# Kernel tuning notes

Measured on AMD Instinct MI355X. Metric: run time of the kernel, lower is better.

The kernel has to match this reference:

```python
import jax, jax.numpy as jnp
import numpy as np

D = 1024
H = 16
HD = D // H
COND = 128
MLP = 4 * D
B, S = 4, 1024
LN_EPS = 1e-5


def _layer_norm(x, w):
    # fp32 LayerNorm (no bias), then scale by weight, matching custom LayerNorm
    xf = x.astype(jnp.float32)
    mu = jnp.mean(xf, axis=-1, keepdims=True)
    var = jnp.mean(jnp.square(xf - mu), axis=-1, keepdims=True)
    y = (xf - mu) * jax.lax.rsqrt(var + LN_EPS)
    return y * w[None, None, :]


def _modulate(x, shift, scale):
    # shift/scale: [B, D] -> broadcast over seq
    return x * (1.0 + scale[:, None, :]) + shift[:, None, :]


def _rope(t, cos, sin):
    # t: [B,S,H,hd]; cos/sin: [S, hd//2]  (GPT-NeoX half-split rotary)
    c = cos[None, :, None, :]
    s = sin[None, :, None, :]
    t1, t2 = jnp.split(t, 2, axis=-1)
    return jnp.concatenate([t1 * c - t2 * s, t2 * c + t1 * s], axis=-1)


def setup_inputs() -> dict:
    key = jax.random.key(0)
    ks = jax.random.split(key, 12)
    std = 0.02
    inp = {
        "x": jax.random.normal(ks[0], (B, S, D), dtype=jnp.float32),
        "c": jax.random.normal(ks[1], (B, COND), dtype=jnp.float32),
        "norm1_w": jnp.ones((D,), dtype=jnp.float32),
        "norm2_w": jnp.ones((D,), dtype=jnp.float32),
        "w_qkv": jax.random.normal(ks[2], (D, 3 * D), dtype=jnp.float32) * std,
        "w_out": jax.random.normal(ks[3], (D, D), dtype=jnp.float32) * std,
        "w1": jax.random.normal(ks[4], (D, MLP), dtype=jnp.float32) * std,
        "b1": jnp.zeros((MLP,), dtype=jnp.float32),
        "w2": jax.random.normal(ks[5], (MLP, D), dtype=jnp.float32) * std,
        "b2": jnp.zeros((D,), dtype=jnp.float32),
        "adaLN_w": jax.random.normal(ks[6], (COND, 6 * D), dtype=jnp.float32) * std,
        "adaLN_b": jnp.zeros((6 * D,), dtype=jnp.float32),
    }
    # rotary tables: cos/sin [S, hd//2]
    inv_freq = 1.0 / (10000.0 ** (jnp.arange(0, HD, 2, dtype=jnp.float32) / HD))
    t = jnp.arange(S, dtype=jnp.float32)
    freqs = t[:, None] * inv_freq[None, :]  # [S, hd//2]
    inp["cos"] = jnp.cos(freqs)
    inp["sin"] = jnp.sin(freqs)
    return inp


def reference(x, c, norm1_w, norm2_w, w_qkv, w_out, w1, b1, w2, b2, adaLN_w, adaLN_b, cos, sin):
    b, s, d = x.shape
    hd = 2 * cos.shape[-1]
    h = d // hd

    # adaLN modulation -> 6 chunks of [B, D]
    mod = c @ adaLN_w + adaLN_b
    shift_msa, scale_msa, gate_msa, shift_mlp, scale_mlp, gate_mlp = jnp.split(mod, 6, axis=-1)

    x_skip = x
    xm = _modulate(_layer_norm(x, norm1_w), shift_msa, scale_msa)

    qkv = (xm @ w_qkv).reshape(b, s, 3, h, hd)
    q = _rope(qkv[:, :, 0], cos, sin)
    k = _rope(qkv[:, :, 1], cos, sin)
    v = qkv[:, :, 2]

    scale = 1.0 / jnp.sqrt(jnp.asarray(hd, dtype=x.dtype))
    scores = jnp.einsum("bshd,bthd->bhst", q, k) * scale
    probs = jax.nn.softmax(scores, axis=-1)
    attn = jnp.einsum("bhst,bthd->bshd", probs, v).reshape(b, s, d)

    # bias_dropout_add_scale (inference: dropout off): residual + gate * out
    x = x_skip + gate_msa[:, None, :] * (attn @ w_out)

    xm2 = _modulate(_layer_norm(x, norm2_w), shift_mlp, scale_mlp)
    hdn = jax.nn.gelu(xm2 @ w1 + b1, approximate=True)
    mlp_out = hdn @ w2 + b2
    x = x + gate_mlp[:, None, :] * mlp_out
    return x
```

## Files before the change

### kernel.cpp

```cpp
#include <hip/hip_runtime.h>

typedef unsigned short u16;
typedef unsigned int u32;
typedef short bf16x8 __attribute__((ext_vector_type(8)));
typedef float f32x4 __attribute__((ext_vector_type(4)));

#define DD 1024
#define SS 1024
#define HH 16
#define HDIM 64
#define MODW 6144

__device__ __forceinline__ float b2f(u16 h){ u32 u = ((u32)h)<<16; return __builtin_bit_cast(float,u); }
__device__ __forceinline__ u16 f2b(float f){
  u32 u = __builtin_bit_cast(u32,f);
  return (u16)((u + 0x7fffu + ((u>>16)&1u))>>16);
}
__device__ __forceinline__ u32 cvtpk(float a, float b){
  u32 r; asm("v_cvt_pk_bf16_f32 %0, %1, %2" : "=v"(r) : "v"(a), "v"(b)); return r;
}
__device__ __forceinline__ void gload16(const u16* g, u16* l){
  __builtin_amdgcn_global_load_lds((const __attribute__((address_space(1))) void*)g,
                                   (__attribute__((address_space(3))) void*)l, 16, 0, 0);
}

__global__ void k_zero(float* __restrict__ out){
  int i = blockIdx.x*256 + threadIdx.x;
  ((float4*)out)[i] = make_float4(0.f,0.f,0.f,0.f);
}

__device__ __forceinline__ void tcast_tile(const float* in, u16* out, int K, int N, int bx, int by){
  __shared__ float t[32][33];
  int n0 = bx*32, k0 = by*32;
  int tx = threadIdx.x & 31, ty = threadIdx.x >> 5;
  #pragma unroll
  for (int i=0;i<4;i++){
    int k = k0 + ty + i*8;
    t[ty+i*8][tx] = in[(size_t)k*N + n0 + tx];
  }
  __syncthreads();
  #pragma unroll
  for (int i=0;i<4;i++){
    int n = n0 + ty + i*8;
    out[(size_t)n*K + k0 + tx] = f2b(t[tx][ty+i*8]);
  }
}
__global__ void k_prep(const float* __restrict__ wqkv, const float* __restrict__ wout,
                       const float* __restrict__ w1, const float* __restrict__ w2,
                       u16* __restrict__ wqkvT, u16* __restrict__ woutT,
                       u16* __restrict__ w1T, u16* __restrict__ w2T,
                       const float* __restrict__ c, const float* __restrict__ aw,
                       const float* __restrict__ ab, float* __restrict__ mod){
  int bid = blockIdx.x;
  if (bid < 3072)       tcast_tile(wqkv, wqkvT, 1024, 3072, bid%96,  bid/96);
  else if (bid < 4096){ int t=bid-3072; tcast_tile(wout, woutT, 1024, 1024, t%32, t/32); }
  else if (bid < 8192){ int t=bid-4096; tcast_tile(w1,   w1T,   1024, 4096, t%128,t/128); }
  else if (bid < 12288){int t=bid-8192; tcast_tile(w2,   w2T,   4096, 1024, t%32, t/32); }
  else {
    int t = bid - 12288;
    int n = (t%24)*256 + threadIdx.x;
    int bb = t/24;
    float acc = ab[n];
    #pragma unroll 4
    for (int k=0;k<128;k++) acc += c[bb*128+k]*aw[(size_t)k*MODW + n];
    mod[(size_t)bb*MODW + n] = acc;
  }
}

__global__ void k_ln_mod(const float* __restrict__ x, const float* __restrict__ w,
                         const float* __restrict__ mod, int shc, int scc,
                         u16* __restrict__ out){
  int row = blockIdx.x;
  int b = row >> 10;
  const float* xr = x + (size_t)row*DD;
  float4 v = ((const float4*)xr)[threadIdx.x];
  float s = v.x+v.y+v.z+v.w;
  float sq = v.x*v.x+v.y*v.y+v.z*v.z+v.w*v.w;
  #pragma unroll
  for (int o=32;o;o>>=1){ s += __shfl_xor(s,o); sq += __shfl_xor(sq,o); }
  __shared__ float ls[4], lq[4];
  int wid = threadIdx.x>>6, lane = threadIdx.x&63;
  if (lane==0){ ls[wid]=s; lq[wid]=sq; }
  __syncthreads();
  s = ls[0]+ls[1]+ls[2]+ls[3]; sq = lq[0]+lq[1]+lq[2]+lq[3];
  float mu = s*(1.f/DD);
  float var = sq*(1.f/DD) - mu*mu;
  float rs = rsqrtf(var + 1e-5f);
  int d0 = threadIdx.x*4;
  const float* mb = mod + (size_t)b*MODW;
  float y0 = ((v.x-mu)*rs*w[d0+0])*(1.f+mb[scc+d0+0]) + mb[shc+d0+0];
  float y1 = ((v.y-mu)*rs*w[d0+1])*(1.f+mb[scc+d0+1]) + mb[shc+d0+1];
  float y2 = ((v.z-mu)*rs*w[d0+2])*(1.f+mb[scc+d0+2]) + mb[shc+d0+2];
  float y3 = ((v.w-mu)*rs*w[d0+3])*(1.f+mb[scc+d0+3]) + mb[shc+d0+3];
  uint2 pk;
  pk.x = (u32)f2b(y0) | ((u32)f2b(y1)<<16);
  pk.y = (u32)f2b(y2) | ((u32)f2b(y3)<<16);
  ((uint2*)(out + (size_t)row*DD))[threadIdx.x] = pk;
}

enum { EPI_QKV=0, EPI_GELU=2, EPI_PARTB=5 };

template<int EPI>
__launch_bounds__(512, 2)
__global__ void k_gemm256(const u16* __restrict__ A, const u16* __restrict__ Bt,
                          int M, int N, int K, int kstride,
                          const float* __restrict__ bias,
                          u16* __restrict__ outb,
                          const float* __restrict__ cosb, const float* __restrict__ sinb,
                          u16* __restrict__ qh, u16* __restrict__ kh, u16* __restrict__ vt){
  __shared__ __align__(16) u16 lds[4][2][8192];
  int tid = threadIdx.x, lane = tid & 63;
  int wid = tid >> 6, wr = wid >> 2, wc = wid & 3;
  int bm = blockIdx.x*256, bn = blockIdx.y*256, z = blockIdx.z;
  f32x4 acc[8][4] = {};
  int srow = (tid>>6)*16 + (tid&15);
  int skk  = ((tid>>4)&3)*8;
  const u16* pa = A  + (size_t)(bm+srow)*kstride + (size_t)z*K + skk;
  const u16* pb = Bt + (size_t)(bn+srow)*kstride + (size_t)z*K + skk;
  size_t rh = (size_t)128*kstride;
  int nk = K >> 5;
  #pragma unroll
  for (int t=0; t<3; ++t){
    gload16(pa + t*32,      &lds[t][0][tid*8]);
    gload16(pa + rh + t*32, &lds[t][0][4096 + tid*8]);
    gload16(pb + t*32,      &lds[t][1][tid*8]);
    gload16(pb + rh + t*32, &lds[t][1][4096 + tid*8]);
  }
  for (int t=0; t<nk; ++t){
    const u16* lA = &lds[t&3][0][0];
    const u16* lB = &lds[t&3][1][0];
    int ahead = nk-1-t;
    if (ahead >= 2)      asm volatile("s_waitcnt vmcnt(8)" ::: "memory");
    else if (ahead == 1) asm volatile("s_waitcnt vmcnt(4)" ::: "memory");
    else                 asm volatile("s_waitcnt vmcnt(0)" ::: "memory");
    __builtin_amdgcn_s_barrier();
    __builtin_amdgcn_sched_barrier(0);
    if (t+3 < nk){
      int u = t+3;
      gload16(pa + u*32,      &lds[u&3][0][tid*8]);
      gload16(pa + rh + u*32, &lds[u&3][0][4096 + tid*8]);
      gload16(pb + u*32,      &lds[u&3][1][tid*8]);
      gload16(pb + rh + u*32, &lds[u&3][1][4096 + tid*8]);
    }
    __builtin_amdgcn_s_setprio(1);
    bf16x8 fa[8], fb[4];
    #pragma unroll
    for (int mi=0;mi<8;mi++) fa[mi] = *(const bf16x8*)(lA + ((wr*8+mi)*64 + lane)*8);
    #pragma unroll
    for (int ni=0;ni<4;ni++) fb[ni] = *(const bf16x8*)(lB + ((wc*4+ni)*64 + lane)*8);
    #pragma unroll
    for (int mi=0;mi<8;mi++)
      #pragma unroll
      for (int ni=0;ni<4;ni++)
        acc[mi][ni] = __builtin_amdgcn_mfma_f32_16x16x32_bf16(fa[mi], fb[ni], acc[mi][ni], 0,0,0);
    __builtin_amdgcn_s_setprio(0);
  }
  int ln = lane & 15;
  int rbase = bm + wr*128 + ((lane>>4)<<2);
  if (EPI == EPI_QKV){
    int cbg = bn + wc*64;
    int ii = cbg >> 10;
    int hh = (cbg >> 6) & 15;
    if (ii == 2){
      #pragma unroll
      for (int mi=0;mi<8;mi++){
        int row = rbase + mi*16;
        int s = row & 1023, b = row >> 10;
        size_t ob = (size_t)(b*16+hh)*65536;
        #pragma unroll
        for (int ni=0;ni<4;ni++){
          int d = ni*16 + ln;
          u32 lo = (u32)f2b(acc[mi][ni][0]) | ((u32)f2b(acc[mi][ni][1])<<16);
          u32 hi = (u32)f2b(acc[mi][ni][2]) | ((u32)f2b(acc[mi][ni][3])<<16);
          *(uint2*)(vt + ob + (size_t)d*1024 + s) = make_uint2(lo,hi);
        }
      }
    } else {
      u16* dst = (ii==0) ? qh : kh;
      float qs = (ii==0) ? 0.125f : 1.0f;
      #pragma unroll
      for (int mi=0;mi<8;mi++){
        #pragma unroll
        for (int r=0;r<4;r++){
          int row = rbase + mi*16 + r;
          int s = row & 1023, b = row >> 10;
          size_t ob = ((size_t)(b*16+hh)*1024 + s)*64;
          #pragma unroll
          for (int ni=0;ni<2;ni++){
            int dlow = ni*16 + ln;
            float cc = cosb[s*32 + dlow], sn = sinb[s*32 + dlow];
            float t1 = acc[mi][ni][r], t2 = acc[mi][ni+2][r];
            dst[ob + dlow]      = f2b((t1*cc - t2*sn)*qs);
            dst[ob + dlow + 32] = f2b((t2*cc + t1*sn)*qs);
          }
        }
      }
    }
    return;
  }
  if (EPI == EPI_PARTB){
    u16* po = outb + (size_t)z*M*N;
    #pragma unroll
    for (int mi=0;mi<8;mi++)
      #pragma unroll
      for (int ni=0;ni<4;ni++){
        int col = bn + wc*64 + ni*16 + ln;
        #pragma unroll
        for (int r=0;r<4;r++)
          po[(size_t)(rbase+mi*16+r)*N + col] = f2b(acc[mi][ni][r]);
      }
    return;
  }
  #pragma unroll
  for (int mi=0;mi<8;mi++)
    #pragma unroll
    for (int ni=0;ni<4;ni++){
      int col = bn + wc*64 + ni*16 + ln;
      float bb = bias[col];
      #pragma unroll
      for (int r=0;r<4;r++){
        float t = acc[mi][ni][r] + bb;
        float y = 0.7978845608f*(t + 0.044715f*t*t*t);
        y = fminf(fmaxf(y, -15.f), 15.f);
        float e = __expf(2.f*y);
        float g = 0.5f*t*(1.f + (e-1.f)/(e+1.f));
        outb[(size_t)(rbase+mi*16+r)*N + col] = f2b(g);
      }
    }
}

__global__ void k_red_ln(const u16* __restrict__ part, const float* __restrict__ x,
                         const float* __restrict__ mod, const float* __restrict__ w,
                         float* __restrict__ x2, u16* __restrict__ act){
  int row = blockIdx.x;
  int b = row >> 10;
  int tid = threadIdx.x;
  int col = tid*4;
  size_t base = (size_t)row*DD + col;
  const size_t MN = (size_t)4096*1024;
  float4 ps = make_float4(0.f,0.f,0.f,0.f);
  #pragma unroll
  for (int z=0; z<4; z++){
    uint2 p = *(const uint2*)(part + (size_t)z*MN + base);
    ps.x += b2f((u16)p.x); ps.y += b2f((u16)(p.x>>16));
    ps.z += b2f((u16)p.y); ps.w += b2f((u16)(p.y>>16));
  }
  const float* mb = mod + (size_t)b*MODW;
  float4 g = *(const float4*)(mb + 2*DD + col);
  float4 rr = *(const float4*)(x + base);
  float4 v;
  v.x = rr.x + g.x*ps.x;
  v.y = rr.y + g.y*ps.y;
  v.z = rr.z + g.z*ps.z;
  v.w = rr.w + g.w*ps.w;
  *(float4*)(x2 + base) = v;
  float s = v.x+v.y+v.z+v.w;
  float sq = v.x*v.x+v.y*v.y+v.z*v.z+v.w*v.w;
  #pragma unroll
  for (int o=32;o;o>>=1){ s += __shfl_xor(s,o); sq += __shfl_xor(sq,o); }
  __shared__ float ls[4], lq[4];
  int wid = tid>>6, lane = tid&63;
  if (lane==0){ ls[wid]=s; lq[wid]=sq; }
  __syncthreads();
  s = ls[0]+ls[1]+ls[2]+ls[3]; sq = lq[0]+lq[1]+lq[2]+lq[3];
  float mu = s*(1.f/DD);
  float var = sq*(1.f/DD) - mu*mu;
  float rs = rsqrtf(var + 1e-5f);
  float y0 = ((v.x-mu)*rs*w[col+0])*(1.f+mb[4*DD+col+0]) + mb[3*DD+col+0];
  float y1 = ((v.y-mu)*rs*w[col+1])*(1.f+mb[4*DD+col+1]) + mb[3*DD+col+1];
  float y2 = ((v.z-mu)*rs*w[col+2])*(1.f+mb[4*DD+col+2]) + mb[3*DD+col+2];
  float y3 = ((v.w-mu)*rs*w[col+3])*(1.f+mb[4*DD+col+3]) + mb[3*DD+col+3];
  uint2 pk;
  pk.x = (u32)f2b(y0) | ((u32)f2b(y1)<<16);
  pk.y = (u32)f2b(y2) | ((u32)f2b(y3)<<16);
  *(uint2*)(act + base) = pk;
}

__global__ void k_reduce4b(const u16* __restrict__ part, size_t MN,
                           const float* __restrict__ resid,
                           const float* __restrict__ mod, int gate_off,
                           const float* __restrict__ bias,
                           float* __restrict__ out){
  int i = blockIdx.x*256 + threadIdx.x;
  int e = i<<2;
  int col = e & 1023;
  int row = e >> 10;
  int b = row >> 10;
  float4 s = make_float4(0.f,0.f,0.f,0.f);
  #pragma unroll
  for (int z=0; z<4; z++){
    uint2 p = ((const uint2*)(part + (size_t)z*MN))[i];
    s.x += b2f((u16)p.x); s.y += b2f((u16)(p.x>>16));
    s.z += b2f((u16)p.y); s.w += b2f((u16)(p.y>>16));
  }
  float4 bb = *(const float4*)(bias + col);
  s.x+=bb.x; s.y+=bb.y; s.z+=bb.z; s.w+=bb.w;
  float4 g = *(const float4*)(mod + (size_t)b*MODW + gate_off + col);
  float4 rr = ((const float4*)resid)[i];
  float4 o;
  o.x = rr.x + g.x*s.x; o.y = rr.y + g.y*s.y;
  o.z = rr.z + g.z*s.z; o.w = rr.w + g.w*s.w;
  ((float4*)out)[i] = o;
}

__launch_bounds__(256, 4)
__global__ void k_attn(const u16* __restrict__ qh, const u16* __restrict__ kh,
                       const u16* __restrict__ vt, u16* __restrict__ attn){
  int blk = blockIdx.x;
  int bh = blk >> 4;
  int qt = blk & 15;
  int tid = threadIdx.x, lane = tid&63, wid = tid>>6;
  int ln = lane&15, kg = lane>>4;
  int sw = ln & 7;
  __shared__ __align__(16) u16 KV[2][2][4096];
  const size_t hb = (size_t)bh*SS*HDIM;

  int qrow = qt*64 + wid*16 + ln;
  const u16* qp = qh + hb + (size_t)qrow*64 + kg*8;
  bf16x8 qf0 = *(const bf16x8*)qp;
  bf16x8 qf1 = *(const bf16x8*)(qp + 32);

  int w0i = wid*64 + lane, w1i = w0i + 256;
  int r0 = w0i>>3, sl0 = (w0i&7) ^ (r0&7);
  int r1 = w1i>>3, sl1 = (w1i&7) ^ (r1&7);
  const u16* gk0 = kh + hb + (size_t)r0*64 + sl0*8;
  const u16* gk1 = kh + hb + (size_t)r1*64 + sl1*8;
  const u16* gv0 = vt + hb + (size_t)r0*1024 + sl0*8;
  const u16* gv1 = vt + hb + (size_t)r1*1024 + sl1*8;

  float mrun = -1e30f, lrun = 0.f;
  f32x4 oc[4] = {};

  gload16(gk0, &KV[0][0][w0i*8]);
  gload16(gk1, &KV[0][0][w1i*8]);
  gload16(gv0, &KV[0][1][w0i*8]);
  gload16(gv1, &KV[0][1][w1i*8]);

  for (int kt=0; kt<16; ++kt){
    int buf = kt & 1;
    __builtin_amdgcn_s_barrier();
    asm volatile("" ::: "memory");
    if (kt < 15){
      int u = kt+1;
      gload16(gk0 + u*4096, &KV[buf^1][0][w0i*8]);
      gload16(gk1 + u*4096, &KV[buf^1][0][w1i*8]);
      gload16(gv0 + u*64,   &KV[buf^1][1][w0i*8]);
      gload16(gv1 + u*64,   &KV[buf^1][1][w1i*8]);
      asm volatile("s_waitcnt vmcnt(4)" ::: "memory");
    } else {
      asm volatile("s_waitcnt vmcnt(0)" ::: "memory");
    }
    __builtin_amdgcn_s_barrier();
    const u16* Kb = KV[buf][0];
    const u16* Vb = KV[buf][1];

    f32x4 sc[4];
    #pragma unroll
    for (int c=0;c<4;c++){
      const u16* kr = Kb + (c*16+ln)*64;
      bf16x8 kf0 = *(const bf16x8*)(kr + (((kg  )^sw)<<3));
      bf16x8 kf1 = *(const bf16x8*)(kr + (((kg+4)^sw)<<3));
      f32x4 zz = {};
      zz   = __builtin_amdgcn_mfma_f32_16x16x32_bf16(kf0, qf0, zz, 0,0,0);
      sc[c]= __builtin_amdgcn_mfma_f32_16x16x32_bf16(kf1, qf1, zz, 0,0,0);
    }
    float mx = fmaxf(fmaxf(fmaxf(sc[0][0],sc[0][1]),fmaxf(sc[0][2],sc[0][3])),
                     fmaxf(fmaxf(sc[1][0],sc[1][1]),fmaxf(sc[1][2],sc[1][3])));
    float mx2= fmaxf(fmaxf(fmaxf(sc[2][0],sc[2][1]),fmaxf(sc[2][2],sc[2][3])),
                     fmaxf(fmaxf(sc[3][0],sc[3][1]),fmaxf(sc[3][2],sc[3][3])));
    mx = fmaxf(mx, mx2);
    mx = fmaxf(mx, __shfl_xor(mx, 16));
    mx = fmaxf(mx, __shfl_xor(mx, 32));
    float mn = fmaxf(mrun, mx);
    float al = __expf(mrun - mn);
    mrun = mn;
    u32 pk[4][2];
    float sum = 0.f;
    #pragma unroll
    for (int c=0;c<4;c++){
      float p0 = __expf(sc[c][0]-mn), p1 = __expf(sc[c][1]-mn);
      float p2 = __expf(sc[c][2]-mn), p3 = __expf(sc[c][3]-mn);
      sum += (p0+p1)+(p2+p3);
      pk[c][0] = cvtpk(p0,p1);
      pk[c][1] = cvtpk(p2,p3);
    }
    sum += __shfl_xor(sum, 16);
    sum += __shfl_xor(sum, 32);
    lrun = lrun*al + sum;
    float alr0 = __shfl(al, kg*4+0), alr1 = __shfl(al, kg*4+1);
    float alr2 = __shfl(al, kg*4+2), alr3 = __shfl(al, kg*4+3);
    #pragma unroll
    for (int c=0;c<4;c++){ oc[c][0]*=alr0; oc[c][1]*=alr1; oc[c][2]*=alr2; oc[c][3]*=alr3; }
    int srcA = ((kg&1)<<5) + ln;
    int hi = kg >> 1;
    #pragma unroll
    for (int kc=0;kc<2;kc++){
      u32 a0 = (u32)__shfl((int)pk[2*kc  ][0], srcA   ), b0 = (u32)__shfl((int)pk[2*kc+1][0], srcA   );
      u32 a1 = (u32)__shfl((int)pk[2*kc  ][1], srcA   ), b1 = (u32)__shfl((int)pk[2*kc+1][1], srcA   );
      u32 a2 = (u32)__shfl((int)pk[2*kc  ][0], srcA+16), b2 = (u32)__shfl((int)pk[2*kc+1][0], srcA+16);
      u32 a3 = (u32)__shfl((int)pk[2*kc  ][1], srcA+16), b3 = (u32)__shfl((int)pk[2*kc+1][1], srcA+16);
      uint4 wv = make_uint4(hi? b0:a0, hi? b1:a1, hi? b2:a2, hi? b3:a3);
      bf16x8 af = __builtin_bit_cast(bf16x8, wv);
      #pragma unroll
      for (int c=0;c<4;c++){
        const u16* vr = Vb + (c*16+ln)*64;
        bf16x8 vf = *(const bf16x8*)(vr + (((kg+4*kc)^sw)<<3));
        oc[c] = __builtin_amdgcn_mfma_f32_16x16x32_bf16(af, vf, oc[c], 0,0,0);
      }
    }
  }
  int b = bh >> 4, h = bh & 15;
  float linv[4];
  linv[0] = 1.f/__shfl(lrun, kg*4+0); linv[1] = 1.f/__shfl(lrun, kg*4+1);
  linv[2] = 1.f/__shfl(lrun, kg*4+2); linv[3] = 1.f/__shfl(lrun, kg*4+3);
  #pragma unroll
  for (int r=0;r<4;r++){
    int srow = qt*64 + wid*16 + kg*4 + r;
    u16* op = attn + (size_t)(b*1024+srow)*DD + h*64;
    #pragma unroll
    for (int c=0;c<4;c++) op[c*16+ln] = f2b(oc[c][r]*linv[r]);
  }
}

extern "C" void kernel_launch(void* const* d_in, const int* in_sizes, int n_in,
                              void* d_out, int out_size, void* d_ws, size_t ws_size,
                              hipStream_t stream){
  const float* x   = (const float*)d_in[0];
  const float* c   = (const float*)d_in[1];
  const float* n1w = (const float*)d_in[2];
  const float* n2w = (const float*)d_in[3];
  const float* wqkv= (const float*)d_in[4];
  const float* wout= (const float*)d_in[5];
  const float* w1  = (const float*)d_in[6];
  const float* b1  = (const float*)d_in[7];
  const float* w2  = (const float*)d_in[8];
  const float* b2  = (const float*)d_in[9];
  const float* aw  = (const float*)d_in[10];
  const float* ab  = (const float*)d_in[11];
  const float* cosb= (const float*)d_in[12];
  const float* sinb= (const float*)d_in[13];

  const size_t REQ = 117538816;
  if (ws_size < REQ){
    k_zero<<<4096,256,0,stream>>>((float*)d_out);
    return;
  }
  char* ws = (char*)d_ws;
  u16*   wqkvT = (u16*)(ws + 0);
  u16*   woutT = (u16*)(ws + 6291456);
  u16*   act   = (u16*)(ws + 8388608);
  float* mod   = (float*)(ws + 16777216);
  float* x2    = (float*)(ws + 16875520);
  u16*   qh    = (u16*)(ws + 16875520);
  u16*   kh    = (u16*)(ws + 25264128);
  u16*   vt    = (u16*)(ws + 33652736);
  u16*   part2b= (u16*)(ws + 33652736);
  u16*   hbuf  = (u16*)(ws + 33652736);
  u16*   w1T   = (u16*)(ws + 67207168);
  u16*   w2T   = (u16*)(ws + 75595776);
  u16*   part4b= (u16*)(ws + 83984384);

  k_prep<<<12384,256,0,stream>>>(wqkv, wout, w1, w2, wqkvT, woutT, w1T, w2T, c, aw, ab, mod);
  k_ln_mod<<<4096,256,0,stream>>>(x, n1w, mod, 0*DD, 1*DD, act);
  k_gemm256<EPI_QKV ><<<dim3(16,12,1),512,0,stream>>>(act, wqkvT, 4096,3072,1024,1024,
        nullptr, nullptr, cosb, sinb, qh, kh, vt);
  k_attn<<<1024,256,0,stream>>>(qh, kh, vt, act);
  k_gemm256<EPI_PARTB><<<dim3(16,4,4),512,0,stream>>>(act, woutT, 4096,1024,256,1024,
        nullptr, part2b, nullptr, nullptr, nullptr, nullptr, nullptr);
  k_red_ln<<<4096,256,0,stream>>>(part2b, x, mod, n2w, x2, act);
  k_gemm256<EPI_GELU><<<dim3(16,16,1),512,0,stream>>>(act, w1T, 4096,4096,1024,1024,
        b1, hbuf, nullptr, nullptr, nullptr, nullptr, nullptr);
  k_gemm256<EPI_PARTB><<<dim3(16,4,4),512,0,stream>>>(hbuf, w2T, 4096,1024,1024,4096,
        nullptr, part4b, nullptr, nullptr, nullptr, nullptr, nullptr);
  k_reduce4b<<<4096,256,0,stream>>>(part4b, (size_t)4096*1024, x2, mod, 5*DD, b2, (float*)d_out);
}
```

Baseline: 362.8 us.

## Restructure GEMM main loop into double-buffered 4-phase interleaved load/MFMA schedule

Replaces the 4-stage LDS ring buffer (one K=32 slice per stage) in the 256x256 GEMM with double-buffered K=64 tiles split into separate A and B buffers. Each K tile is processed in four phases that interleave LDS fragment reads, next-tile global-to-LDS loads, and quarter-sized MFMA bursts with explicit barriers and waitcnts. The aim is to overlap memory traffic with MFMA work at finer granularity and cut register pressure for fragments. It adds many more barriers per iteration and a shallower prefetch depth, which could expose global load latency.

```diff
diff --git a/kernel.cpp b/kernel.cpp
--- a/kernel.cpp
+++ b/kernel.cpp
@@ -100,6 +100,33 @@
 
 enum { EPI_QKV=0, EPI_GELU=2, EPI_PARTB=5 };
 
+#define BARR  __builtin_amdgcn_s_barrier()
+#define LGKM0 asm volatile("s_waitcnt lgkmcnt(0)" ::: "memory")
+#define SB0   __builtin_amdgcn_sched_barrier(0)
+#define VMC(n) asm volatile("s_waitcnt vmcnt(" #n ")" ::: "memory")
+
+#define STG_A(bf, kt, kh) do{ const u16* _s = pa + (kt)*64 + (kh)*32; \
+  gload16(_s,      &Als[bf][kh][tid*8]); \
+  gload16(_s + rh, &Als[bf][kh][(512+tid)*8]); }while(0)
+#define STG_B(bf, kt, kh) do{ const u16* _s = pb + (kt)*64 + (kh)*32; \
+  gload16(_s,      &Bls[bf][kh][tid*8]); \
+  gload16(_s + rh, &Bls[bf][kh][(512+tid)*8]); }while(0)
+
+#define LDA4(bf, kh, mlo) do{ const u16* _b = &Als[bf][kh][0]; \
+  _Pragma("unroll") \
+  for (int m=0;m<4;m++) av[m] = *(const bf16x8*)(_b + ((wr*8+(mlo)+m)*64 + lane)*8); }while(0)
+#define LDB4(bf, kh) do{ const u16* _b = &Bls[bf][kh][0]; \
+  _Pragma("unroll") \
+  for (int n=0;n<4;n++) bv[n] = *(const bf16x8*)(_b + ((wc*4+n)*64 + lane)*8); }while(0)
+
+#define MMQ4(mlo) do{ __builtin_amdgcn_s_setprio(1); \
+  _Pragma("unroll") \
+  for (int m=0;m<4;m++){ \
+    _Pragma("unroll") \
+    for (int n=0;n<4;n++) \
+      acc[(mlo)+m][n] = __builtin_amdgcn_mfma_f32_16x16x32_bf16(av[m], bv[n], acc[(mlo)+m][n], 0,0,0); } \
+  __builtin_amdgcn_s_setprio(0); }while(0)
+
 template<int EPI>
 __launch_bounds__(512, 2)
 __global__ void k_gemm256(const u16* __restrict__ A, const u16* __restrict__ Bt,
@@ -108,7 +135,8 @@
                           u16* __restrict__ outb,
                           const float* __restrict__ cosb, const float* __restrict__ sinb,
                           u16* __restrict__ qh, u16* __restrict__ kh, u16* __restrict__ vt){
-  __shared__ __align__(16) u16 lds[4][2][8192];
+  __shared__ __align__(16) u16 Als[2][2][8192];
+  __shared__ __align__(16) u16 Bls[2][2][8192];
   int tid = threadIdx.x, lane = tid & 63;
   int wid = tid >> 6, wr = wid >> 2, wc = wid & 3;
   int bm = blockIdx.x*256, bn = blockIdx.y*256, z = blockIdx.z;
@@ -118,42 +146,41 @@
   const u16* pa = A  + (size_t)(bm+srow)*kstride + (size_t)z*K + skk;
   const u16* pb = Bt + (size_t)(bn+srow)*kstride + (size_t)z*K + skk;
   size_t rh = (size_t)128*kstride;
-  int nk = K >> 5;
-  #pragma unroll
-  for (int t=0; t<3; ++t){
-    gload16(pa + t*32,      &lds[t][0][tid*8]);
-    gload16(pa + rh + t*32, &lds[t][0][4096 + tid*8]);
-    gload16(pb + t*32,      &lds[t][1][tid*8]);
-    gload16(pb + rh + t*32, &lds[t][1][4096 + tid*8]);
-  }
-  for (int t=0; t<nk; ++t){
-    const u16* lA = &lds[t&3][0][0];
-    const u16* lB = &lds[t&3][1][0];
-    int ahead = nk-1-t;
-    if (ahead >= 2)      asm volatile("s_waitcnt vmcnt(8)" ::: "memory");
-    else if (ahead == 1) asm volatile("s_waitcnt vmcnt(4)" ::: "memory");
-    else                 asm volatile("s_waitcnt vmcnt(0)" ::: "memory");
-    __builtin_amdgcn_s_barrier();
-    __builtin_amdgcn_sched_barrier(0);
-    if (t+3 < nk){
-      int u = t+3;
-      gload16(pa + u*32,      &lds[u&3][0][tid*8]);
-      gload16(pa + rh + u*32, &lds[u&3][0][4096 + tid*8]);
-      gload16(pb + u*32,      &lds[u&3][1][tid*8]);
-      gload16(pb + rh + u*32, &lds[u&3][1][4096 + tid*8]);
-    }
-    __builtin_amdgcn_s_setprio(1);
-    bf16x8 fa[8], fb[4];
-    #pragma unroll
-    for (int mi=0;mi<8;mi++) fa[mi] = *(const bf16x8*)(lA + ((wr*8+mi)*64 + lane)*8);
-    #pragma unroll
-    for (int ni=0;ni<4;ni++) fb[ni] = *(const bf16x8*)(lB + ((wc*4+ni)*64 + lane)*8);
-    #pragma unroll
-    for (int mi=0;mi<8;mi++)
-      #pragma unroll
-      for (int ni=0;ni<4;ni++)
-        acc[mi][ni] = __builtin_amdgcn_mfma_f32_16x16x32_bf16(fa[mi], fb[ni], acc[mi][ni], 0,0,0);
-    __builtin_amdgcn_s_setprio(0);
+  int nkt = K >> 6;
+  bf16x8 av[4], bv[4];
+
+  STG_A(0, 0, 0);
+  STG_B(0, 0, 0);
+  STG_A(0, 0, 1);
+  STG_B(0, 0, 1);
+  VMC(4);
+  BARR; SB0;
+
+  for (int kt=0; kt<nkt; ++kt){
+    int bf = kt & 1;
+    bool nx = (kt+1 < nkt);
+    LDA4(bf, 0, 0); LDB4(bf, 0);
+    if (nx) STG_A(bf^1, kt+1, 0);
+    BARR; LGKM0; SB0;
+    MMQ4(0);
+    BARR; SB0;
+    LDA4(bf, 0, 4);
+    if (nx) STG_B(bf^1, kt+1, 0);
+    BARR; LGKM0; SB0;
+    MMQ4(4);
+    if (nx) VMC(4); else VMC(0);
+    BARR; SB0;
+    LDA4(bf, 1, 0); LDB4(bf, 1);
+    if (nx) STG_A(bf^1, kt+1, 1);
+    BARR; LGKM0; SB0;
+    MMQ4(0);
+    BARR; SB0;
+    LDA4(bf, 1, 4);
+    if (nx) STG_B(bf^1, kt+1, 1);
+    BARR; LGKM0; SB0;
+    MMQ4(4);
+    if (nx) VMC(4);
+    BARR; SB0;
   }
   int ln = lane & 15;
   int rbase = bm + wr*128 + ((lane>>4)<<2);
```

New measurement: 374.2 us. 1.03x slower.

## Shrink GEMM tile to 256x128 with XCD-aware block remap and 3-stage buffer

Applied to the files above, without the earlier changes.

The shared GEMM kernel drops from a 256x256 tile to 256x128, with each wave holding a 64x64 accumulator instead of 128x64. The LDS pipeline goes from 4 stages to 3, and launch bounds now request 4 blocks per SM. Block indices are remapped so that neighbouring tiles land on the same XCD, which should improve L2 reuse. This doubles the grid sizes and aims for more occupancy and better tail balance, at the cost of lower arithmetic intensity per tile and a shallower prefetch.

```diff
diff --git a/kernel.cpp b/kernel.cpp
--- a/kernel.cpp
+++ b/kernel.cpp
@@ -100,70 +100,74 @@
 
 enum { EPI_QKV=0, EPI_GELU=2, EPI_PARTB=5 };
 
+#define VMC(n) asm volatile("s_waitcnt vmcnt(" #n ")" ::: "memory")
+
 template<int EPI>
-__launch_bounds__(512, 2)
+__launch_bounds__(512, 4)
 __global__ void k_gemm256(const u16* __restrict__ A, const u16* __restrict__ Bt,
                           int M, int N, int K, int kstride,
                           const float* __restrict__ bias,
                           u16* __restrict__ outb,
                           const float* __restrict__ cosb, const float* __restrict__ sinb,
                           u16* __restrict__ qh, u16* __restrict__ kh, u16* __restrict__ vt){
-  __shared__ __align__(16) u16 lds[4][2][8192];
+  __shared__ __align__(16) u16 Ab[3][8192];
+  __shared__ __align__(16) u16 Bb[3][4096];
   int tid = threadIdx.x, lane = tid & 63;
-  int wid = tid >> 6, wr = wid >> 2, wc = wid & 3;
-  int bm = blockIdx.x*256, bn = blockIdx.y*256, z = blockIdx.z;
-  f32x4 acc[8][4] = {};
+  int wid = tid >> 6, wr = wid >> 1, wc = wid & 1;
+  int g   = blockIdx.y * gridDim.x + blockIdx.x;
+  int xcd = g & 7, slot = g >> 3;
+  int gy2 = gridDim.y >> 1;
+  int bxp = (xcd >> 1)*4 + (slot & 3);
+  int byp = (xcd & 1)*gy2 + (slot >> 2);
+  int bm = bxp*256, bn = byp*128, z = blockIdx.z;
+  f32x4 acc[4][4] = {};
   int srow = (tid>>6)*16 + (tid&15);
   int skk  = ((tid>>4)&3)*8;
   const u16* pa = A  + (size_t)(bm+srow)*kstride + (size_t)z*K + skk;
   const u16* pb = Bt + (size_t)(bn+srow)*kstride + (size_t)z*K + skk;
   size_t rh = (size_t)128*kstride;
   int nk = K >> 5;
-  #pragma unroll
-  for (int t=0; t<3; ++t){
-    gload16(pa + t*32,      &lds[t][0][tid*8]);
-    gload16(pa + rh + t*32, &lds[t][0][4096 + tid*8]);
-    gload16(pb + t*32,      &lds[t][1][tid*8]);
-    gload16(pb + rh + t*32, &lds[t][1][4096 + tid*8]);
-  }
+  gload16(pa,           &Ab[0][tid*8]);
+  gload16(pa + rh,      &Ab[0][(512+tid)*8]);
+  gload16(pb,           &Bb[0][tid*8]);
+  gload16(pa + 32,      &Ab[1][tid*8]);
+  gload16(pa + rh + 32, &Ab[1][(512+tid)*8]);
+  gload16(pb + 32,      &Bb[1][tid*8]);
   for (int t=0; t<nk; ++t){
-    const u16* lA = &lds[t&3][0][0];
-    const u16* lB = &lds[t&3][1][0];
-    int ahead = nk-1-t;
-    if (ahead >= 2)      asm volatile("s_waitcnt vmcnt(8)" ::: "memory");
-    else if (ahead == 1) asm volatile("s_waitcnt vmcnt(4)" ::: "memory");
-    else                 asm volatile("s_waitcnt vmcnt(0)" ::: "memory");
+    if (t+1 < nk) VMC(3); else VMC(0);
     __builtin_amdgcn_s_barrier();
     __builtin_amdgcn_sched_barrier(0);
-    if (t+3 < nk){
-      int u = t+3;
-      gload16(pa + u*32,      &lds[u&3][0][tid*8]);
-      gload16(pa + rh + u*32, &lds[u&3][0][4096 + tid*8]);
-      gload16(pb + u*32,      &lds[u&3][1][tid*8]);
-      gload16(pb + rh + u*32, &lds[u&3][1][4096 + tid*8]);
-    }
+    if (t+2 < nk){
+      int bf = (t+2)%3;
+      const u16* s = pa + (t+2)*32;
+      gload16(s,              &Ab[bf][tid*8]);
+      gload16(s + rh,         &Ab[bf][(512+tid)*8]);
+      gload16(pb + (t+2)*32,  &Bb[bf][tid*8]);
+    }
+    const u16* lA = &Ab[t%3][0];
+    const u16* lB = &Bb[t%3][0];
     __builtin_amdgcn_s_setprio(1);
-    bf16x8 fa[8], fb[4];
-    #pragma unroll
-    for (int mi=0;mi<8;mi++) fa[mi] = *(const bf16x8*)(lA + ((wr*8+mi)*64 + lane)*8);
+    bf16x8 fa[4], fb[4];
+    #pragma unroll
+    for (int mi=0;mi<4;mi++) fa[mi] = *(const bf16x8*)(lA + ((wr*4+mi)*64 + lane)*8);
     #pragma unroll
     for (int ni=0;ni<4;ni++) fb[ni] = *(const bf16x8*)(lB + ((wc*4+ni)*64 + lane)*8);
     #pragma unroll
-    for (int mi=0;mi<8;mi++)
+    for (int mi=0;mi<4;mi++)
       #pragma unroll
       for (int ni=0;ni<4;ni++)
         acc[mi][ni] = __builtin_amdgcn_mfma_f32_16x16x32_bf16(fa[mi], fb[ni], acc[mi][ni], 0,0,0);
     __builtin_amdgcn_s_setprio(0);
   }
   int ln = lane & 15;
-  int rbase = bm + wr*128 + ((lane>>4)<<2);
+  int rbase = bm + wr*64 + ((lane>>4)<<2);
   if (EPI == EPI_QKV){
     int cbg = bn + wc*64;
     int ii = cbg >> 10;
     int hh = (cbg >> 6) & 15;
     if (ii == 2){
       #pragma unroll
-      for (int mi=0;mi<8;mi++){
+      for (int mi=0;mi<4;mi++){
         int row = rbase + mi*16;
         int s = row & 1023, b = row >> 10;
         size_t ob = (size_t)(b*16+hh)*65536;
@@ -179,7 +183,7 @@
       u16* dst = (ii==0) ? qh : kh;
       float qs = (ii==0) ? 0.125f : 1.0f;
       #pragma unroll
-      for (int mi=0;mi<8;mi++){
+      for (int mi=0;mi<4;mi++){
         #pragma unroll
         for (int r=0;r<4;r++){
           int row = rbase + mi*16 + r;
@@ -201,7 +205,7 @@
   if (EPI == EPI_PARTB){
     u16* po = outb + (size_t)z*M*N;
     #pragma unroll
-    for (int mi=0;mi<8;mi++)
+    for (int mi=0;mi<4;mi++)
       #pragma unroll
       for (int ni=0;ni<4;ni++){
         int col = bn + wc*64 + ni*16 + ln;
@@ -212,7 +216,7 @@
     return;
   }
   #pragma unroll
-  for (int mi=0;mi<8;mi++)
+  for (int mi=0;mi<4;mi++)
     #pragma unroll
     for (int ni=0;ni<4;ni++){
       int col = bn + wc*64 + ni*16 + ln;
@@ -223,8 +227,8 @@
         float y = 0.7978845608f*(t + 0.044715f*t*t*t);
         y = fminf(fmaxf(y, -15.f), 15.f);
         float e = __expf(2.f*y);
-        float g = 0.5f*t*(1.f + (e-1.f)/(e+1.f));
-        outb[(size_t)(rbase+mi*16+r)*N + col] = f2b(g);
+        float g2 = 0.5f*t*(1.f + (e-1.f)/(e+1.f));
+        outb[(size_t)(rbase+mi*16+r)*N + col] = f2b(g2);
       }
     }
 }
@@ -462,15 +466,15 @@
 
   k_prep<<<12384,256,0,stream>>>(wqkv, wout, w1, w2, wqkvT, woutT, w1T, w2T, c, aw, ab, mod);
   k_ln_mod<<<4096,256,0,stream>>>(x, n1w, mod, 0*DD, 1*DD, act);
-  k_gemm256<EPI_QKV ><<<dim3(16,12,1),512,0,stream>>>(act, wqkvT, 4096,3072,1024,1024,
+  k_gemm256<EPI_QKV ><<<dim3(16,24,1),512,0,stream>>>(act, wqkvT, 4096,3072,1024,1024,
         nullptr, nullptr, cosb, sinb, qh, kh, vt);
   k_attn<<<1024,256,0,stream>>>(qh, kh, vt, act);
-  k_gemm256<EPI_PARTB><<<dim3(16,4,4),512,0,stream>>>(act, woutT, 4096,1024,256,1024,
+  k_gemm256<EPI_PARTB><<<dim3(16,8,4),512,0,stream>>>(act, woutT, 4096,1024,256,1024,
         nullptr, part2b, nullptr, nullptr, nullptr, nullptr, nullptr);
   k_red_ln<<<4096,256,0,stream>>>(part2b, x, mod, n2w, x2, act);
-  k_gemm256<EPI_GELU><<<dim3(16,16,1),512,0,stream>>>(act, w1T, 4096,4096,1024,1024,
+  k_gemm256<EPI_GELU><<<dim3(16,32,1),512,0,stream>>>(act, w1T, 4096,4096,1024,1024,
         b1, hbuf, nullptr, nullptr, nullptr, nullptr, nullptr);
-  k_gemm256<EPI_PARTB><<<dim3(16,4,4),512,0,stream>>>(hbuf, w2T, 4096,1024,1024,4096,
+  k_gemm256<EPI_PARTB><<<dim3(16,8,4),512,0,stream>>>(hbuf, w2T, 4096,1024,1024,4096,
         nullptr, part4b, nullptr, nullptr, nullptr, nullptr, nullptr);
   k_reduce4b<<<4096,256,0,stream>>>(part4b, (size_t)4096*1024, x2, mod, 5*DD, b2, (float*)d_out);
 }
```

New measurement: 394.7 us. +8.8%, slower.
